# Optimization experiments

Measured on AMD Instinct MI355X. Metric: run time of the kernel, lower is better.

Reference implementation:

```python
import jax, jax.numpy as jnp
import numpy as np

B, J, D, K = 2048, 15, 9, 20
HID, NF = 256, 24


def _linear_params(key, fin, fout):
    kw, kb = jax.random.split(key)
    lim = 1.0 / np.sqrt(fin)
    W = jax.random.uniform(kw, (fin, fout), minval=-lim, maxval=lim, dtype=jnp.float32)
    b = jax.random.uniform(kb, (fout,), minval=-lim, maxval=lim, dtype=jnp.float32)
    return W, b


def setup_inputs() -> dict:
    key = jax.random.key(0)
    ks = jax.random.split(key, 9)
    inp = {"dct_input": jax.random.normal(ks[0], (B, J, D, K), dtype=jnp.float32)}
    inp["q_W1"], inp["q_b1"] = _linear_params(ks[1], K, HID)
    inp["q_W2"], inp["q_b2"] = _linear_params(ks[2], HID, HID)
    inp["k_W1"], inp["k_b1"] = _linear_params(ks[3], K, HID)
    inp["k_W2"], inp["k_b2"] = _linear_params(ks[4], HID, HID)
    inp["v_W1"], inp["v_b1"] = _linear_params(ks[5], K, HID)
    inp["v_W2"], inp["v_b2"] = _linear_params(ks[6], HID, HID)
    inp["p_W1"], inp["p_b1"] = _linear_params(ks[7], 2 * HID, HID)
    inp["p_W2"], inp["p_b2"] = _linear_params(ks[8], HID, NF)
    return inp


def _mlp(x, W1, b1, W2, b2):
    return jax.nn.relu(x @ W1 + b1) @ W2 + b2


def _idct_basis(n):
    # IDCT of DCT-II with norm='ortho' (scipy.fftpack.idct default type=2):
    # x[t] = sum_k c_k * X[k] * cos(pi*k*(2t+1)/(2n)), c_0=sqrt(1/n), c_k=sqrt(2/n)
    k = jnp.arange(n, dtype=jnp.float32)[:, None]
    t = jnp.arange(n, dtype=jnp.float32)[None, :]
    c = jnp.full((n, 1), np.sqrt(2.0 / n), dtype=jnp.float32).at[0, 0].set(np.sqrt(1.0 / n))
    return c * jnp.cos(np.pi * k * (2.0 * t + 1.0) / (2.0 * n))  # [k, t]


def reference(dct_input, q_W1, q_b1, q_W2, q_b2, k_W1, k_b1, k_W2, k_b2,
              v_W1, v_b1, v_W2, v_b2, p_W1, p_b1, p_W2, p_b2):
    b, j, d, kdim = dct_input.shape
    x = dct_input.reshape(b, j * d, kdim)          # tokens = J*D
    Q = _mlp(x, q_W1, q_b1, q_W2, q_b2)            # [B, T, H]
    Kt = _mlp(x, k_W1, k_b1, k_W2, k_b2)
    V = _mlp(x, v_W1, v_b1, v_W2, v_b2)
    scores = jnp.einsum('bth,bsh->bts', Q, Kt) / np.sqrt(Q.shape[-1])
    attn = jax.nn.softmax(scores, axis=-1)
    context = jnp.einsum('bts,bsh->bth', attn, V)
    feat = jnp.concatenate([Q, context], axis=-1)  # [B, T, 2H]
    out = _mlp(feat, p_W1, p_b1, p_W2, p_b2)       # [B, T, NF] (DCT coeffs)
    out = out.reshape(b, j, d, NF).transpose(0, 3, 1, 2)  # [B, NF, J, D]
    M = _idct_basis(NF)                            # [NF(k), NF(t)]
    time = jnp.einsum('bkjd,kt->btjd', out, M)     # inverse DCT along time axis
    pred = time.reshape(b, NF, j, 3, 3)
    return pred
```

## Files before the change

kernel.cpp:

```cpp
#include <hip/hip_runtime.h>

#define BDIM 512

typedef float f32x4 __attribute__((ext_vector_type(4)));
typedef short bf16x8 __attribute__((ext_vector_type(8)));

#define MFMA(a, b, c) __builtin_amdgcn_mfma_f32_16x16x32_bf16((a), (b), (c), 0, 0, 0)

constexpr int OQ1 = 0;
constexpr int OK1w = 8192;
constexpr int OV1 = 16384;
constexpr int OQ2 = 24576;
constexpr int OK2w = 90112;
constexpr int OV2 = 155648;
constexpr int OP1 = 221184;
constexpr int OP2 = 352256;
constexpr int WTOT = 360448;

constexpr int OFF_Q   = 0;
constexpr int OFF_XS  = 73728;
constexpr int OFF_SP  = 83968;
constexpr int OFF_HT2 = 127776;
constexpr int OFF_KVT = 144160;
constexpr int OFF_RWL = 160544;
constexpr int SMEM_BYTES = 161120;

constexpr int SPS = 152;

__device__ __forceinline__ unsigned short f2b(float f) {
  unsigned int u = __float_as_uint(f);
  return (unsigned short)((u + 0x7fffu + ((u >> 16) & 1u)) >> 16);
}
__device__ __forceinline__ float bfu(unsigned short u) {
  return __uint_as_float(((unsigned int)u) << 16);
}

__device__ __forceinline__ bf16x8 frag(const unsigned short* m, int rb, int stride,
                                       int kb, int lane) {
  return *(const bf16x8*)(m + (rb + (lane & 15)) * stride + kb + ((lane >> 4) << 3));
}
__device__ __forceinline__ bf16x8 frag256s(const unsigned short* m, int rb, int kb, int lane) {
  const int row = rb + (lane & 15);
  const int c = (kb + ((lane >> 4) << 3)) ^ ((row & 7) << 3);
  return *(const bf16x8*)(m + row * 256 + c);
}
__device__ __forceinline__ bf16x8 frag32s(const unsigned short* m, int rb, int lane) {
  const int row = rb + (lane & 15);
  const int c = ((lane >> 4) << 3) ^ (((row >> 1) & 3) << 3);
  return *(const bf16x8*)(m + row * 32 + c);
}
__device__ __forceinline__ int swz256(int r, int c) { return r * 256 + (c ^ ((r & 7) << 3)); }
__device__ __forceinline__ int swz32 (int r, int c) { return r * 32  + (c ^ (((r >> 1) & 3) << 3)); }

__global__ void prep_w(const float* __restrict__ qW1, const float* __restrict__ qW2,
                       const float* __restrict__ kW1, const float* __restrict__ kW2,
                       const float* __restrict__ vW1, const float* __restrict__ vW2,
                       const float* __restrict__ pW1, const float* __restrict__ pW2,
                       unsigned short* __restrict__ ws) {
  int i = blockIdx.x * 256 + threadIdx.x;
  if (i >= WTOT) return;
  float v = 0.f;
  if (i < OQ2) {
    int sel = i >> 13, r = i & 8191;
    int o = r >> 5, k = r & 31;
    const float* W = (sel == 0) ? qW1 : (sel == 1) ? kW1 : vW1;
    if (k < 20) v = W[k * 256 + o];
  } else if (i < OP1) {
    int r = i - OQ2;
    int sel = r >> 16, q = r & 65535;
    int o = q >> 8, k = q & 255;
    const float* W = (sel == 0) ? qW2 : (sel == 1) ? kW2 : vW2;
    v = W[k * 256 + o];
  } else if (i < OP2) {
    int r = i - OP1;
    int o = r >> 9, f = r & 511;
    v = pW1[f * 256 + o];
  } else {
    int r = i - OP2;
    int o = r >> 8, k = r & 255;
    if (o < 24) v = pW2[k * 24 + o];
  }
  ws[i] = f2b(v);
}

__global__ __launch_bounds__(BDIM) __attribute__((amdgpu_waves_per_eu(2, 2)))
void motion_mfma(const float* __restrict__ x,
                 const float* __restrict__ qb1v, const float* __restrict__ qb2v,
                 const float* __restrict__ kb1v, const float* __restrict__ kb2v,
                 const float* __restrict__ vb1v, const float* __restrict__ vb2v,
                 const float* __restrict__ pb1v, const float* __restrict__ pb2v,
                 const unsigned short* __restrict__ ws,
                 float* __restrict__ out) {
  extern __shared__ char smem[];
  unsigned short* Qs  = (unsigned short*)(smem + OFF_Q);
  unsigned short* XS  = (unsigned short*)(smem + OFF_XS);
  unsigned short* SP  = (unsigned short*)(smem + OFF_SP);
  unsigned short* Hc  = (unsigned short*)(smem + OFF_SP);
  unsigned short* HT2 = (unsigned short*)(smem + OFF_HT2);
  unsigned short* KVT = (unsigned short*)(smem + OFF_KVT);
  float* RWL = (float*)(smem + OFF_RWL);
  float* Ob  = (float*)(smem + 0);
  float* MT  = (float*)(smem + 14400);

  const int tid = threadIdx.x, lane = tid & 63, w = tid >> 6;
  const int l15 = lane & 15, rs = ((lane >> 4) << 2);
  const int cb = w * 32;
  const int b = blockIdx.x;
  const f32x4 zf4 = {0.f, 0.f, 0.f, 0.f};
  const bf16x8 zb8 = {0, 0, 0, 0, 0, 0, 0, 0};

  const float* xb = x + (size_t)b * 2700;
  for (int i = tid; i < 160 * 32; i += BDIM) {
    int r = i >> 5, c = i & 31;
    float v = (r < 135 && c < 20) ? __builtin_nontemporal_load(xb + r * 20 + c) : 0.f;
    XS[swz32(r, c)] = f2b(v);
  }

  const bf16x8 kw0 = frag(ws + OK1w, cb, 32, 0, lane);
  const bf16x8 kw1 = frag(ws + OK1w, cb + 16, 32, 0, lane);
  const bf16x8 vw0 = frag(ws + OV1, cb, 32, 0, lane);
  const bf16x8 vw1 = frag(ws + OV1, cb + 16, 32, 0, lane);
  const float kbb0 = kb1v[cb + l15], kbb1 = kb1v[cb + 16 + l15];
  const float vbb0 = vb1v[cb + l15], vbb1 = vb1v[cb + 16 + l15];
  __syncthreads();

  auto L1 = [&](const bf16x8& u0, const bf16x8& u1, float bb0, float bb1, int s0) {
#pragma unroll
    for (int mm = 0; mm < 2; ++mm) {
      bf16x8 a = frag32s(XS, s0 + mm * 16, lane);
      f32x4 c0 = MFMA(a, u0, zf4), c1 = MFMA(a, u1, zf4);
#pragma unroll
      for (int r = 0; r < 4; ++r) {
        HT2[swz256(mm * 16 + rs + r, cb + l15)]      = f2b(fmaxf(c0[r] + bb0, 0.f));
        HT2[swz256(mm * 16 + rs + r, cb + 16 + l15)] = f2b(fmaxf(c1[r] + bb1, 0.f));
      }
    }
  };

  {
    bf16x8 w0 = frag(ws + OQ1, cb, 32, 0, lane);
    bf16x8 w1 = frag(ws + OQ1, cb + 16, 32, 0, lane);
    float bb0 = qb1v[cb + l15], bb1 = qb1v[cb + 16 + l15];
#pragma unroll
    for (int m = 0; m < 9; ++m) {
      bf16x8 a = frag32s(XS, m * 16, lane);
      f32x4 c0 = MFMA(a, w0, zf4);
      f32x4 c1 = MFMA(a, w1, zf4);
#pragma unroll
      for (int r = 0; r < 4; ++r) {
        Hc[swz256(m * 16 + rs + r, cb + l15)]      = f2b(fmaxf(c0[r] + bb0, 0.f));
        Hc[swz256(m * 16 + rs + r, cb + 16 + l15)] = f2b(fmaxf(c1[r] + bb1, 0.f));
      }
    }
  }
  __syncthreads();

  {
    f32x4 acc[9][2];
#pragma unroll
    for (int m = 0; m < 9; ++m) { acc[m][0] = zf4; acc[m][1] = zf4; }
#pragma unroll
    for (int ks = 0; ks < 8; ++ks) {
      bf16x8 g0 = frag(ws + OQ2, cb, 256, ks * 32, lane);
      bf16x8 g1 = frag(ws + OQ2, cb + 16, 256, ks * 32, lane);
#pragma unroll
      for (int m = 0; m < 9; ++m) {
        bf16x8 a = frag256s(Hc, m * 16, ks * 32, lane);
        acc[m][0] = MFMA(a, g0, acc[m][0]);
        acc[m][1] = MFMA(a, g1, acc[m][1]);
      }
    }
    float bb20 = qb2v[cb + l15], bb21 = qb2v[cb + 16 + l15];
#pragma unroll
    for (int m = 0; m < 9; ++m)
#pragma unroll
      for (int r = 0; r < 4; ++r) {
        Qs[swz256(m * 16 + rs + r, cb + l15)]      = f2b(acc[m][0][r] + bb20);
        Qs[swz256(m * 16 + rs + r, cb + 16 + l15)] = f2b(acc[m][1][r] + bb21);
      }
  }
  __syncthreads();

  L1(kw0, kw1, kbb0, kbb1, 0);
  __syncthreads();

  bf16x8 kg[8][2];
#pragma unroll
  for (int ks = 0; ks < 8; ++ks) {
    kg[ks][0] = frag(ws + OK2w, cb, 256, ks * 32, lane);
    kg[ks][1] = frag(ws + OK2w, cb + 16, 256, ks * 32, lane);
  }

  for (int ch = 0; ch < 5; ++ch) {
    const int s0 = ch * 32;
    {
      f32x4 a2[2][2] = {{zf4, zf4}, {zf4, zf4}};
#pragma unroll
      for (int ks = 0; ks < 8; ++ks) {
#pragma unroll
        for (int mm = 0; mm < 2; ++mm) {
          bf16x8 a = frag256s(HT2, mm * 16, ks * 32, lane);
          a2[mm][0] = MFMA(a, kg[ks][0], a2[mm][0]);
          a2[mm][1] = MFMA(a, kg[ks][1], a2[mm][1]);
        }
      }
      float bb0 = kb2v[cb + l15], bb1 = kb2v[cb + 16 + l15];
#pragma unroll
      for (int mm = 0; mm < 2; ++mm)
#pragma unroll
        for (int r = 0; r < 4; ++r) {
          KVT[swz256(mm * 16 + rs + r, cb + l15)]      = f2b(a2[mm][0][r] + bb0);
          KVT[swz256(mm * 16 + rs + r, cb + 16 + l15)] = f2b(a2[mm][1][r] + bb1);
        }
    }
    __syncthreads();
    if (ch < 4) L1(kw0, kw1, kbb0, kbb1, s0 + 32);
    else        L1(vw0, vw1, vbb0, vbb1, 0);
#pragma unroll
    for (int rep = 0; rep < 3; ++rep) {
      int j = w + rep * 8;
      if (j < 18) {
        int m = j >> 1, n = j & 1;
        int sb = s0 + n * 16;
        if (sb < 144) {
          f32x4 sa = zf4;
#pragma unroll
          for (int ks = 0; ks < 8; ++ks) {
            bf16x8 qa = frag256s(Qs, m * 16, ks * 32, lane);
            bf16x8 kf = frag256s(KVT, n * 16, ks * 32, lane);
            sa = MFMA(qa, kf, sa);
          }
#pragma unroll
          for (int r = 0; r < 4; ++r)
            SP[(m * 16 + rs + r) * SPS + sb + l15] = f2b(sa[r] * 0.0625f);
        }
      }
    }
    __syncthreads();
  }

#pragma unroll
  for (int pass = 0; pass < 2; ++pass) {
    int r = pass * 128 + (tid >> 2);
    if (r < 144) {
      int j = tid & 3;
      float mx = -1e30f;
      for (int s = j; s < 135; s += 4) mx = fmaxf(mx, bfu(SP[r * SPS + s]));
      mx = fmaxf(mx, __shfl_xor(mx, 1));
      mx = fmaxf(mx, __shfl_xor(mx, 2));
      float sum = 0.f;
      for (int s = j; s < 135; s += 4) {
        float p = __expf(bfu(SP[r * SPS + s]) - mx);
        SP[r * SPS + s] = f2b(p);
        sum += p;
      }
      sum += __shfl_xor(sum, 1);
      sum += __shfl_xor(sum, 2);
      if (j == 0) RWL[r] = sum;
      for (int s = 135 + j; s < 144; s += 4) SP[r * SPS + s] = 0;
    }
  }
  __syncthreads();

  bf16x8 vg[8][2];
#pragma unroll
  for (int ks = 0; ks < 8; ++ks) {
    vg[ks][0] = frag(ws + OV2, cb, 256, ks * 32, lane);
    vg[ks][1] = frag(ws + OV2, cb + 16, 256, ks * 32, lane);
  }

  f32x4 ctx[9][2];
#pragma unroll
  for (int m = 0; m < 9; ++m) { ctx[m][0] = zf4; ctx[m][1] = zf4; }
  for (int ch = 0; ch < 5; ++ch) {
    const int s0 = ch * 32;
    {
      f32x4 a2[2][2] = {{zf4, zf4}, {zf4, zf4}};
#pragma unroll
      for (int ks = 0; ks < 8; ++ks) {
#pragma unroll
        for (int mm = 0; mm < 2; ++mm) {
          bf16x8 a = frag256s(HT2, mm * 16, ks * 32, lane);
          a2[mm][0] = MFMA(a, vg[ks][0], a2[mm][0]);
          a2[mm][1] = MFMA(a, vg[ks][1], a2[mm][1]);
        }
      }
      float bb0 = vb2v[cb + l15], bb1 = vb2v[cb + 16 + l15];
#pragma unroll
      for (int mm = 0; mm < 2; ++mm)
#pragma unroll
        for (int r = 0; r < 4; ++r) {
          KVT[swz32(cb + l15,      mm * 16 + rs + r)] = f2b(a2[mm][0][r] + bb0);
          KVT[swz32(cb + 16 + l15, mm * 16 + rs + r)] = f2b(a2[mm][1][r] + bb1);
        }
    }
    __syncthreads();
    if (ch < 4) L1(vw0, vw1, vbb0, vbb1, s0 + 32);
    {
      bf16x8 v0 = frag32s(KVT, cb, lane);
      bf16x8 v1 = frag32s(KVT, cb + 16, lane);
      const bool mask = (ch == 4) && (lane >= 32);
#pragma unroll
      for (int m = 0; m < 9; ++m) {
        bf16x8 pa = frag(SP, m * 16, SPS, s0, lane);
        if (mask) pa = zb8;
        ctx[m][0] = MFMA(pa, v0, ctx[m][0]);
        ctx[m][1] = MFMA(pa, v1, ctx[m][1]);
      }
    }
    __syncthreads();
  }

#pragma unroll
  for (int m = 0; m < 9; ++m)
#pragma unroll
    for (int r = 0; r < 4; ++r) {
      int t = m * 16 + rs + r;
      float inv = 1.0f / RWL[t];
      Hc[swz256(t, cb + l15)]      = f2b(ctx[m][0][r] * inv);
      Hc[swz256(t, cb + 16 + l15)] = f2b(ctx[m][1][r] * inv);
    }
  __syncthreads();

  {
    float pbias0 = pb1v[cb + l15], pbias1 = pb1v[cb + 16 + l15];
    f32x4 pacc[9][2];
#pragma unroll
    for (int m = 0; m < 9; ++m) {
      pacc[m][0] = (f32x4){pbias0, pbias0, pbias0, pbias0};
      pacc[m][1] = (f32x4){pbias1, pbias1, pbias1, pbias1};
    }
#pragma unroll
    for (int ks = 0; ks < 8; ++ks) {
      bf16x8 g0 = frag(ws + OP1, cb, 512, ks * 32, lane);
      bf16x8 g1 = frag(ws + OP1, cb + 16, 512, ks * 32, lane);
#pragma unroll
      for (int m = 0; m < 9; ++m) {
        bf16x8 a = frag256s(Qs, m * 16, ks * 32, lane);
        pacc[m][0] = MFMA(a, g0, pacc[m][0]);
        pacc[m][1] = MFMA(a, g1, pacc[m][1]);
      }
    }
#pragma unroll
    for (int ks = 0; ks < 8; ++ks) {
      bf16x8 g0 = frag(ws + OP1, cb, 512, 256 + ks * 32, lane);
      bf16x8 g1 = frag(ws + OP1, cb + 16, 512, 256 + ks * 32, lane);
#pragma unroll
      for (int m = 0; m < 9; ++m) {
        bf16x8 a = frag256s(Hc, m * 16, ks * 32, lane);
        pacc[m][0] = MFMA(a, g0, pacc[m][0]);
        pacc[m][1] = MFMA(a, g1, pacc[m][1]);
      }
    }
    __syncthreads();
#pragma unroll
    for (int m = 0; m < 9; ++m)
#pragma unroll
      for (int r = 0; r < 4; ++r) {
        Hc[swz256(m * 16 + rs + r, cb + l15)]      = f2b(fmaxf(pacc[m][0][r], 0.f));
        Hc[swz256(m * 16 + rs + r, cb + 16 + l15)] = f2b(fmaxf(pacc[m][1][r], 0.f));
      }
  }
  for (int i = tid; i < 576; i += BDIM) {
    int kk = i / 24, t = i - kk * 24;
    float c = (kk == 0) ? 0.20412414523193150f : 0.28867513459481287f;
    MT[i] = c * cosf(0.065449846949787352f * (float)(kk * (2 * t + 1)));
  }
  __syncthreads();

#pragma unroll
  for (int rep = 0; rep < 3; ++rep) {
    int j = w + rep * 8;
    if (j < 18) {
      int m = j >> 1, n = j & 1;
      f32x4 oa = zf4;
#pragma unroll
      for (int ks = 0; ks < 8; ++ks) {
        bf16x8 a = frag256s(Hc, m * 16, ks * 32, lane);
        bf16x8 g = frag(ws + OP2, n * 16, 256, ks * 32, lane);
        oa = MFMA(a, g, oa);
      }
      int c = n * 16 + l15;
      if (c < 24) {
        float bb = pb2v[c];
#pragma unroll
        for (int r = 0; r < 4; ++r)
          Ob[(m * 16 + rs + r) * 25 + c] = oa[r] + bb;
      }
    }
  }
  __syncthreads();

  for (int i = tid; i < 3240; i += BDIM) {
    int tt = i / 135, tok = i - tt * 135;
    float a = 0.f;
#pragma unroll
    for (int k = 0; k < 24; ++k)
      a = fmaf(Ob[tok * 25 + k], MT[k * 24 + tt], a);
    __builtin_nontemporal_store(a, out + (size_t)b * 3240 + i);
  }
}

extern "C" void kernel_launch(void* const* d_in, const int* in_sizes, int n_in,
                              void* d_out, int out_size, void* d_ws, size_t ws_size,
                              hipStream_t stream) {
  (void)in_sizes; (void)n_in; (void)out_size;
  if (ws_size < (size_t)WTOT * 2) return;

  const float* x   = (const float*)d_in[0];
  const float* qW1 = (const float*)d_in[1];
  const float* qb1 = (const float*)d_in[2];
  const float* qW2 = (const float*)d_in[3];
  const float* qb2 = (const float*)d_in[4];
  const float* kW1 = (const float*)d_in[5];
  const float* kb1 = (const float*)d_in[6];
  const float* kW2 = (const float*)d_in[7];
  const float* kb2 = (const float*)d_in[8];
  const float* vW1 = (const float*)d_in[9];
  const float* vb1 = (const float*)d_in[10];
  const float* vW2 = (const float*)d_in[11];
  const float* vb2 = (const float*)d_in[12];
  const float* pW1 = (const float*)d_in[13];
  const float* pb1 = (const float*)d_in[14];
  const float* pW2 = (const float*)d_in[15];
  const float* pb2 = (const float*)d_in[16];
  float* out = (float*)d_out;
  unsigned short* ws = (unsigned short*)d_ws;

  prep_w<<<dim3((WTOT + 255) / 256), dim3(256), 0, stream>>>(
      qW1, qW2, kW1, kW2, vW1, vW2, pW1, pW2, ws);

  (void)hipFuncSetAttribute((const void*)motion_mfma,
                            hipFuncAttributeMaxDynamicSharedMemorySize, SMEM_BYTES);
  motion_mfma<<<dim3(2048), dim3(BDIM), SMEM_BYTES, stream>>>(
      x, qb1, qb2, kb1, kb2, vb1, vb2, pb1, pb2, ws, out);
}
```

Before: 588.5 us.

## Fold V second-layer weights into projection weights, skip per-block V2 GEMM

Since the attention rows sum to one, context = attn·(relu(xW1+b1)·W2 + b2) can be rewritten so the V second-layer matrix and its bias are folded into the context half of the projection's first layer (W2·pW1_ctx) and into the projection bias. A small prep kernel computes the folded weights and bias into the workspace. The main kernel then attends over the V hidden layer directly, double-buffering it in LDS, and drops the per-chunk 256x256 V GEMM, one barrier per chunk and the vg register fragments. In exchange, the folded weights are rounded to bf16 and the fold reorders floating-point work.

```diff
diff --git a/kernel.cpp b/kernel.cpp
--- a/kernel.cpp
+++ b/kernel.cpp
@@ -83,6 +83,27 @@
   ws[i] = f2b(v);
 }
 
+__global__ void g3_prep(const float* __restrict__ vW2, const float* __restrict__ pW1,
+                        const float* __restrict__ pb1, const float* __restrict__ vb2,
+                        unsigned short* __restrict__ ws) {
+  __shared__ float col[256];
+  __shared__ float red[256];
+  const int o = blockIdx.x, c = threadIdx.x;
+  col[c] = pW1[(256 + c) * 256 + o];
+  __syncthreads();
+  float acc = 0.f;
+#pragma unroll 4
+  for (int h = 0; h < 256; ++h) acc += vW2[c * 256 + h] * col[h];
+  ws[OP1 + o * 512 + 256 + c] = f2b(acc);
+  red[c] = vb2[c] * col[c];
+  __syncthreads();
+  for (int st = 128; st > 0; st >>= 1) {
+    if (c < st) red[c] += red[c + st];
+    __syncthreads();
+  }
+  if (c == 0) ((float*)(ws + OV2))[o] = pb1[o] + red[0];
+}
+
 __global__ __launch_bounds__(BDIM) __attribute__((amdgpu_waves_per_eu(2, 2)))
 void motion_mfma(const float* __restrict__ x,
                  const float* __restrict__ qb1v, const float* __restrict__ qb2v,
@@ -98,6 +119,8 @@
   unsigned short* Hc  = (unsigned short*)(smem + OFF_SP);
   unsigned short* HT2 = (unsigned short*)(smem + OFF_HT2);
   unsigned short* KVT = (unsigned short*)(smem + OFF_KVT);
+  unsigned short* VB0 = (unsigned short*)(smem + OFF_HT2);
+  unsigned short* VB1 = (unsigned short*)(smem + OFF_KVT);
   float* RWL = (float*)(smem + OFF_RWL);
   float* Ob  = (float*)(smem + 0);
   float* MT  = (float*)(smem + 14400);
@@ -136,6 +159,19 @@
       }
     }
   };
+  auto L1T = [&](int s0, unsigned short* buf) {
+#pragma unroll
+    for (int mm = 0; mm < 2; ++mm) {
+      bf16x8 a = frag32s(XS, s0 + mm * 16, lane);
+      f32x4 c0 = MFMA(a, vw0, zf4), c1 = MFMA(a, vw1, zf4);
+#pragma unroll
+      for (int r = 0; r < 4; ++r) {
+        int tok = mm * 16 + rs + r;
+        buf[swz32(cb + l15,      tok)] = f2b(fmaxf(c0[r] + vbb0, 0.f));
+        buf[swz32(cb + 16 + l15, tok)] = f2b(fmaxf(c1[r] + vbb1, 0.f));
+      }
+    }
+  };
 
   {
     bf16x8 w0 = frag(ws + OQ1, cb, 32, 0, lane);
@@ -215,7 +251,7 @@
     }
     __syncthreads();
     if (ch < 4) L1(kw0, kw1, kbb0, kbb1, s0 + 32);
-    else        L1(vw0, vw1, vbb0, vbb1, 0);
+    else        L1T(0, VB0);
 #pragma unroll
     for (int rep = 0; rep < 3; ++rep) {
       int j = w + rep * 8;
@@ -262,43 +298,17 @@
   }
   __syncthreads();
 
-  bf16x8 vg[8][2];
-#pragma unroll
-  for (int ks = 0; ks < 8; ++ks) {
-    vg[ks][0] = frag(ws + OV2, cb, 256, ks * 32, lane);
-    vg[ks][1] = frag(ws + OV2, cb + 16, 256, ks * 32, lane);
-  }
-
   f32x4 ctx[9][2];
 #pragma unroll
   for (int m = 0; m < 9; ++m) { ctx[m][0] = zf4; ctx[m][1] = zf4; }
   for (int ch = 0; ch < 5; ++ch) {
     const int s0 = ch * 32;
+    const unsigned short* rd = (ch & 1) ? VB1 : VB0;
+    unsigned short* wr = (ch & 1) ? VB0 : VB1;
+    if (ch < 4) L1T(s0 + 32, wr);
     {
-      f32x4 a2[2][2] = {{zf4, zf4}, {zf4, zf4}};
-#pragma unroll
-      for (int ks = 0; ks < 8; ++ks) {
-#pragma unroll
-        for (int mm = 0; mm < 2; ++mm) {
-          bf16x8 a = frag256s(HT2, mm * 16, ks * 32, lane);
-          a2[mm][0] = MFMA(a, vg[ks][0], a2[mm][0]);
-          a2[mm][1] = MFMA(a, vg[ks][1], a2[mm][1]);
-        }
-      }
-      float bb0 = vb2v[cb + l15], bb1 = vb2v[cb + 16 + l15];
-#pragma unroll
-      for (int mm = 0; mm < 2; ++mm)
-#pragma unroll
-        for (int r = 0; r < 4; ++r) {
-          KVT[swz32(cb + l15,      mm * 16 + rs + r)] = f2b(a2[mm][0][r] + bb0);
-          KVT[swz32(cb + 16 + l15, mm * 16 + rs + r)] = f2b(a2[mm][1][r] + bb1);
-        }
-    }
-    __syncthreads();
-    if (ch < 4) L1(vw0, vw1, vbb0, vbb1, s0 + 32);
-    {
-      bf16x8 v0 = frag32s(KVT, cb, lane);
-      bf16x8 v1 = frag32s(KVT, cb + 16, lane);
+      bf16x8 v0 = frag32s(rd, cb, lane);
+      bf16x8 v1 = frag32s(rd, cb + 16, lane);
       const bool mask = (ch == 4) && (lane >= 32);
 #pragma unroll
       for (int m = 0; m < 9; ++m) {
@@ -323,7 +333,8 @@
   __syncthreads();
 
   {
-    float pbias0 = pb1v[cb + l15], pbias1 = pb1v[cb + 16 + l15];
+    const float* pb1adj = (const float*)(ws + OV2);
+    float pbias0 = pb1adj[cb + l15], pbias1 = pb1adj[cb + 16 + l15];
     f32x4 pacc[9][2];
 #pragma unroll
     for (int m = 0; m < 9; ++m) {
@@ -429,6 +440,7 @@
 
   prep_w<<<dim3((WTOT + 255) / 256), dim3(256), 0, stream>>>(
       qW1, qW2, kW1, kW2, vW1, vW2, pW1, pW2, ws);
+  g3_prep<<<dim3(256), dim3(256), 0, stream>>>(vW2, pW1, pb1, vb2, ws);
 
   (void)hipFuncSetAttribute((const void*)motion_mfma,
                             hipFuncAttributeMaxDynamicSharedMemorySize, SMEM_BYTES);
```

New measurement: 539.5 us. 8.3% less time.
